# Kernel optimization log

Hardware: AMD Instinct MI355X
Metric: run time of the kernel (lower is better)

## Reference

```python
import jax, jax.numpy as jnp
import numpy as np

B, S, D = 2, 2048, 768
E, TOP_K = 8, 2
H = 4 * D  # expert hidden dim


def setup_inputs() -> dict:
    key = jax.random.key(0)
    ks = jax.random.split(key, 8)
    s_in = 1.0 / np.sqrt(D)
    s_h = 1.0 / np.sqrt(H)
    return {
        "x": jax.random.normal(ks[0], (B, S, D), dtype=jnp.float32),
        "gate_w": jax.random.uniform(ks[1], (D, E), jnp.float32, -s_in, s_in),
        "gate_b": jax.random.uniform(ks[2], (E,), jnp.float32, -s_in, s_in),
        "w1": jax.random.uniform(ks[3], (E, D, H), jnp.float32, -s_in, s_in),
        "b1": jax.random.uniform(ks[4], (E, H), jnp.float32, -s_in, s_in),
        "w2": jax.random.uniform(ks[5], (E, H, D), jnp.float32, -s_h, s_h),
        "b2": jax.random.uniform(ks[6], (E, D), jnp.float32, -s_h, s_h),
    }


def reference(x, gate_w, gate_b, w1, b1, w2, b2):
    # Router: gate linear -> top-k -> softmax over the k selected logits
    logits = jnp.einsum("bsd,de->bse", x, gate_w) + gate_b          # [B,S,E]
    top_vals, top_idx = jax.lax.top_k(logits, TOP_K)                 # [B,S,K]
    rw = jax.nn.softmax(top_vals, axis=-1)                           # [B,S,K]
    # Per-token per-expert combine weight (0 for unselected experts)
    onehot = jax.nn.one_hot(top_idx, E, dtype=x.dtype)               # [B,S,K,E]
    expert_w = jnp.einsum("bske,bsk->bse", onehot, rw)               # [B,S,E]

    # Expert MLPs (GELU exact, matching torch nn.GELU default; dropout is
    # identity in eval). Stacked as grouped GEMMs over the expert axis.
    h = jax.nn.gelu(jnp.einsum("bsd,edh->bseh", x, w1) + b1, approximate=False)
    y = jnp.einsum("bseh,ehd->bsed", h, w2) + b2                     # [B,S,E,D]
    # Weighted combine over experts
    return jnp.einsum("bse,bsed->bsd", expert_w, y)                  # [B,S,D]
```

## Files before the change

kernel.cpp:

```cpp
#include <hip/hip_runtime.h>
#include <hip/hip_bf16.h>

#define D_ 768
#define E_ 8
#define H_ 3072
#define N_TOK 4096
#define BT 64
#define BK 64

typedef _Float16 f16;
typedef f16 f16x8 __attribute__((ext_vector_type(8)));
typedef float f32x4 __attribute__((ext_vector_type(4)));

__device__ __forceinline__ void gld16(const f16* g, f16* l) {
    __builtin_amdgcn_global_load_lds(
        (const __attribute__((address_space(1))) unsigned int*)g,
        (__attribute__((address_space(3))) unsigned int*)l, 16, 0, 0);
}

__device__ __forceinline__ int prefix_off(const int* counts, int e, int* cnt_out) {
    int off = 0, cnt = 0;
#pragma unroll
    for (int q = 0; q < E_; q++) {
        int cq = counts[q];
        if (q < e) off += cq;
        if (q == e) cnt = cq;
    }
    *cnt_out = cnt;
    return off;
}

__global__ __launch_bounds__(1024) void router(const float* __restrict__ x,
                                               const float* __restrict__ gw,
                                               const float* __restrict__ gb,
                                               int* __restrict__ counts,
                                               int* __restrict__ list,
                                               float* __restrict__ wslot) {
    __shared__ int lcount[E_];
    __shared__ int lbase[E_];
    __shared__ int te0[64], te1[64], ts0[64], ts1[64];
    __shared__ float tw0[64], tw1[64];

    int tid = threadIdx.x;
    int wv = tid >> 6, lane = tid & 63;
    int s = lane >> 3, eL = lane & 7;
    if (tid < E_) lcount[tid] = 0;
    __syncthreads();

    float biasL = gb[eL];

#pragma unroll 1
    for (int i = 0; i < 4; i++) {
        int lt = wv * 4 + i;
        int tok = blockIdx.x * 64 + lt;
        const float* xr = x + (size_t)tok * D_;
        float a = 0.f;
        const float* gwl = gw + lane;
#pragma unroll 8
        for (int j = 0; j < 96; j++)
            a = fmaf(xr[j * 8 + s], gwl[j * 64], a);
        a += __shfl_xor(a, 8, 64);
        a += __shfl_xor(a, 16, 64);
        a += __shfl_xor(a, 32, 64);
        float lg = a + biasL;
        float le[8];
#pragma unroll
        for (int q = 0; q < 8; q++) le[q] = __shfl(lg, q, 64);
        float v0 = -3.4e38f, v1 = -3.4e38f;
        int i0 = 0, i1 = 0;
#pragma unroll
        for (int q = 0; q < 8; q++) {
            float l = le[q];
            if (l > v0) { v1 = v0; i1 = i0; v0 = l; i0 = q; }
            else if (l > v1) { v1 = l; i1 = q; }
        }
        if (lane == 0) {
            float p1 = expf(v1 - v0);
            float ssum = 1.f + p1;
            int s0 = atomicAdd(&lcount[i0], 1);
            int s1 = atomicAdd(&lcount[i1], 1);
            te0[lt] = i0; ts0[lt] = s0; tw0[lt] = 1.f / ssum;
            te1[lt] = i1; ts1[lt] = s1; tw1[lt] = p1 / ssum;
        }
    }
    __syncthreads();
    if (tid < E_) lbase[tid] = atomicAdd(&counts[tid], lcount[tid]);
    __syncthreads();
    if (tid < 64) {
        int tok = blockIdx.x * 64 + tid;
        int e0 = te0[tid], e1 = te1[tid];
        list[e0 * N_TOK + lbase[e0] + ts0[tid]] = tok * 2;
        list[e1 * N_TOK + lbase[e1] + ts1[tid]] = tok * 2 + 1;
        wslot[tok * 2] = tw0[tid];
        wslot[tok * 2 + 1] = tw1[tid];
    }
}

#define CVT_BLKS 9216
__global__ __launch_bounds__(256) void prep(const float* __restrict__ w1,
                                            const float* __restrict__ w2,
                                            f16* __restrict__ w1t,
                                            f16* __restrict__ w2t,
                                            const float* __restrict__ x,
                                            const int* __restrict__ counts,
                                            const int* __restrict__ list,
                                            f16* __restrict__ xg) {
    __shared__ f16 t[64][66];
    int bid = blockIdx.x;
    int tid = threadIdx.x;

    if (bid < CVT_BLKS) {
        int z = bid / 576;
        int bx = bid % 576;
        const float* src; f16* dst; int R, C, xb, yb;
        if (z < E_) {
            src = w1 + (size_t)z * D_ * H_; dst = w1t + (size_t)z * D_ * H_;
            R = D_; C = H_; xb = bx % 48; yb = bx / 48;
        } else {
            src = w2 + (size_t)(z - E_) * H_ * D_; dst = w2t + (size_t)(z - E_) * H_ * D_;
            R = H_; C = D_; xb = bx % 12; yb = bx / 12;
        }
        int r0 = yb * 64, c0 = xb * 64;
        {
            int r = tid >> 4;
            int c = (tid & 15) * 4;
#pragma unroll
            for (int i = 0; i < 4; i++) {
                float4 v = *(const float4*)(src + (size_t)(r0 + r + i * 16) * C + (c0 + c));
                t[r + i * 16][c] = (f16)v.x;
                t[r + i * 16][c + 1] = (f16)v.y;
                t[r + i * 16][c + 2] = (f16)v.z;
                t[r + i * 16][c + 3] = (f16)v.w;
            }
        }
        __syncthreads();
        {
            int c = tid >> 3;
            int rr = (tid & 7) * 8;
            int ch = rr >> 3;
#pragma unroll
            for (int i = 0; i < 2; i++) {
                int cc = c + i * 32;
                int rowi = c0 + cc;
                f16x8 o;
#pragma unroll
                for (int j = 0; j < 8; j++) o[j] = t[rr + j][cc];
                *(f16x8*)(dst + (size_t)rowi * R + r0 + (((ch ^ rowi) & 7) << 3)) = o;
            }
        }
    } else {
        int wv = tid >> 6, lane = tid & 63;
        int idx = (bid - CVT_BLKS) * 4 + wv;
        int e = idx >> 12, j = idx & (N_TOK - 1);
        int cnt;
        int off = prefix_off(counts, e, &cnt);
        if (j >= cnt) return;
        int id = list[idx];
        int row = off + j;
        const float* xr = x + (size_t)(id >> 1) * D_;
        f16* dst = xg + (size_t)row * D_;
        int r7 = row & 7;
#pragma unroll
        for (int c = 0; c < 3; c++) {
            int h = lane * 4 + c * 256;
            float4 v = *(const float4*)(xr + h);
            f16 o[4] = {(f16)v.x, (f16)v.y, (f16)v.z, (f16)v.w};
            int hs = (h & ~0x3F) | ((((h >> 3) ^ r7) & 7) << 3) | (h & 7);
            *(float2*)(dst + hs) = *(const float2*)o;
        }
    }
}

__global__ __launch_bounds__(256, 8) void gemm1(const f16* __restrict__ xg,
                                                const f16* __restrict__ w1t,
                                                const float* __restrict__ b1,
                                                const int* __restrict__ counts,
                                                f16* __restrict__ hbuf) {
    int bid = blockIdx.x;
    int e = bid & 7;
    int r = bid >> 3;
    int xb24 = r % 24;
    int yb = (r / 24) % 64;
    int xh = r / (24 * 64);
    int cnt;
    int off = prefix_off(counts, e, &cnt);
    int rb = yb * BT;
    if (rb >= cnt) return;
    int cb = (xh * 24 + xb24) * BT;

    __shared__ f16 lds[2 * BT * BK];
    char* ldsb = (char*)lds;

    int tid = threadIdx.x;
    int wv = tid >> 6, lane = tid & 63;
    int lr = lane >> 3, lc = lane & 7;

    int r0l = wv * 8 + lr;
    int r1l = 32 + wv * 8 + lr;
    int ag0 = off + rb + r0l; if (ag0 > 8191) ag0 = 8191;
    int ag1 = off + rb + r1l; if (ag1 > 8191) ag1 = 8191;
    const f16* ap0 = xg + (size_t)ag0 * D_ + lc * 8;
    const f16* ap1 = xg + (size_t)ag1 * D_ + lc * 8;
    const f16* wb = w1t + (size_t)e * H_ * D_;
    const f16* bp0 = wb + (size_t)(cb + r0l) * D_ + lc * 8;
    const f16* bp1 = wb + (size_t)(cb + r1l) * D_ + lc * 8;
    f16* la0 = lds + wv * 512;
    f16* la1 = lds + 2048 + wv * 512;
    f16* lb0 = lds + 4096 + wv * 512;
    f16* lb1 = lds + 6144 + wv * 512;

    int wr = (wv >> 1) * 32, wc = (wv & 1) * 32;
    int fr = lane & 15, qh = lane >> 4;
    int koff = (off + rb) & 7;

    int roA[2][2], roB[2][2];
#pragma unroll
    for (int m = 0; m < 2; m++)
#pragma unroll
        for (int ks = 0; ks < 2; ks++) {
            int row = wr + m * 16 + fr;
            roA[m][ks] = row * 128 + ((((ks * 4 + qh) ^ (koff + row)) & 7) << 4);
            int rwb = wc + m * 16 + fr;
            roB[m][ks] = 8192 + rwb * 128 + ((((ks * 4 + qh) ^ rwb) & 7) << 4);
        }

    f32x4 acc[2][2] = {};
    const int NT = D_ / BK;
#pragma unroll 1
    for (int t = 0; t < NT; ++t) {
        int kk = t * BK;
        gld16(ap0 + kk, la0);
        gld16(ap1 + kk, la1);
        gld16(bp0 + kk, lb0);
        gld16(bp1 + kk, lb1);
        __syncthreads();
#pragma unroll
        for (int ks = 0; ks < 2; ks++) {
            f16x8 a0 = *(const f16x8*)(ldsb + roA[0][ks]);
            f16x8 a1 = *(const f16x8*)(ldsb + roA[1][ks]);
            f16x8 b0 = *(const f16x8*)(ldsb + roB[0][ks]);
            f16x8 b1v = *(const f16x8*)(ldsb + roB[1][ks]);
            acc[0][0] = __builtin_amdgcn_mfma_f32_16x16x32_f16(a0, b0, acc[0][0], 0, 0, 0);
            acc[0][1] = __builtin_amdgcn_mfma_f32_16x16x32_f16(a0, b1v, acc[0][1], 0, 0, 0);
            acc[1][0] = __builtin_amdgcn_mfma_f32_16x16x32_f16(a1, b0, acc[1][0], 0, 0, 0);
            acc[1][1] = __builtin_amdgcn_mfma_f32_16x16x32_f16(a1, b1v, acc[1][1], 0, 0, 0);
        }
        __syncthreads();
    }

#pragma unroll
    for (int n = 0; n < 2; n++) {
        int colg = cb + wc + n * 16 + fr;
        float bias = b1[e * H_ + colg];
#pragma unroll
        for (int m = 0; m < 2; m++) {
#pragma unroll
            for (int r2 = 0; r2 < 4; r2++) {
                int j = rb + wr + m * 16 + qh * 4 + r2;
                if (j < cnt) {
                    float v = acc[m][n][r2] + bias;
                    v = 0.5f * v * (1.f + erff(v * 0.70710678f));
                    int row = off + j;
                    int hs = (colg & ~0x3F) | ((((colg >> 3) ^ row) & 7) << 3) | (colg & 7);
                    hbuf[(size_t)row * H_ + hs] = (f16)v;
                }
            }
        }
    }
}

__global__ __launch_bounds__(256, 8) void gemm2(const f16* __restrict__ hbuf,
                                                const f16* __restrict__ w2t,
                                                const float* __restrict__ b2,
                                                const int* __restrict__ counts,
                                                const int* __restrict__ list,
                                                const float* __restrict__ wslot,
                                                float* __restrict__ out) {
    int bid = blockIdx.x;
    int e = bid & 7;
    int r = bid >> 3;
    int cb12 = r % 12;
    int yb = r / 12;
    int cnt;
    int off = prefix_off(counts, e, &cnt);
    int rb = yb * BT;
    if (rb >= cnt) return;
    int cb = cb12 * BT;

    __shared__ f16 lds[2 * BT * BK];
    char* ldsb = (char*)lds;

    int tid = threadIdx.x;
    int wv = tid >> 6, lane = tid & 63;
    int lr = lane >> 3, lc = lane & 7;

    int r0l = wv * 8 + lr;
    int r1l = 32 + wv * 8 + lr;
    int ag0 = off + rb + r0l; if (ag0 > 8191) ag0 = 8191;
    int ag1 = off + rb + r1l; if (ag1 > 8191) ag1 = 8191;
    const f16* ap0 = hbuf + (size_t)ag0 * H_ + lc * 8;
    const f16* ap1 = hbuf + (size_t)ag1 * H_ + lc * 8;
    const f16* wb = w2t + (size_t)e * D_ * H_;
    const f16* bp0 = wb + (size_t)(cb + r0l) * H_ + lc * 8;
    const f16* bp1 = wb + (size_t)(cb + r1l) * H_ + lc * 8;
    f16* la0 = lds + wv * 512;
    f16* la1 = lds + 2048 + wv * 512;
    f16* lb0 = lds + 4096 + wv * 512;
    f16* lb1 = lds + 6144 + wv * 512;

    int wr = (wv >> 1) * 32, wc = (wv & 1) * 32;
    int fr = lane & 15, qh = lane >> 4;
    int koff = (off + rb) & 7;

    int roA[2][2], roB[2][2];
#pragma unroll
    for (int m = 0; m < 2; m++)
#pragma unroll
        for (int ks = 0; ks < 2; ks++) {
            int row = wr + m * 16 + fr;
            roA[m][ks] = row * 128 + ((((ks * 4 + qh) ^ (koff + row)) & 7) << 4);
            int rwb = wc + m * 16 + fr;
            roB[m][ks] = 8192 + rwb * 128 + ((((ks * 4 + qh) ^ rwb) & 7) << 4);
        }

    f32x4 acc[2][2] = {};
    const int NT = H_ / BK;
#pragma unroll 1
    for (int t = 0; t < NT; ++t) {
        int kk = t * BK;
        gld16(ap0 + kk, la0);
        gld16(ap1 + kk, la1);
        gld16(bp0 + kk, lb0);
        gld16(bp1 + kk, lb1);
        __syncthreads();
#pragma unroll
        for (int ks = 0; ks < 2; ks++) {
            f16x8 a0 = *(const f16x8*)(ldsb + roA[0][ks]);
            f16x8 a1 = *(const f16x8*)(ldsb + roA[1][ks]);
            f16x8 b0 = *(const f16x8*)(ldsb + roB[0][ks]);
            f16x8 b1v = *(const f16x8*)(ldsb + roB[1][ks]);
            acc[0][0] = __builtin_amdgcn_mfma_f32_16x16x32_f16(a0, b0, acc[0][0], 0, 0, 0);
            acc[0][1] = __builtin_amdgcn_mfma_f32_16x16x32_f16(a0, b1v, acc[0][1], 0, 0, 0);
            acc[1][0] = __builtin_amdgcn_mfma_f32_16x16x32_f16(a1, b0, acc[1][0], 0, 0, 0);
            acc[1][1] = __builtin_amdgcn_mfma_f32_16x16x32_f16(a1, b1v, acc[1][1], 0, 0, 0);
        }
        __syncthreads();
    }

#pragma unroll
    for (int n = 0; n < 2; n++) {
        int colg = cb + wc + n * 16 + fr;
        float bias = b2[e * D_ + colg];
#pragma unroll
        for (int m = 0; m < 2; m++) {
#pragma unroll
            for (int r2 = 0; r2 < 4; r2++) {
                int j = rb + wr + m * 16 + qh * 4 + r2;
                if (j < cnt) {
                    int id = list[e * N_TOK + j];
                    float w = wslot[id];
                    float v = (acc[m][n][r2] + bias) * w;
                    atomicAdd(&out[(size_t)(id >> 1) * D_ + colg], v);
                }
            }
        }
    }
}

extern "C" void kernel_launch(void* const* d_in, const int* in_sizes, int n_in,
                              void* d_out, int out_size, void* d_ws, size_t ws_size,
                              hipStream_t stream) {
    const float* x = (const float*)d_in[0];
    const float* gate_w = (const float*)d_in[1];
    const float* gate_b = (const float*)d_in[2];
    const float* w1 = (const float*)d_in[3];
    const float* b1 = (const float*)d_in[4];
    const float* w2 = (const float*)d_in[5];
    const float* b2 = (const float*)d_in[6];
    float* out = (float*)d_out;

    char* ws = (char*)d_ws;
    int* counts = (int*)ws;
    int* list = (int*)(ws + 1024);
    float* wslot = (float*)(ws + 132096);
    f16* xg = (f16*)(ws + 196608);
    f16* w1t = (f16*)(ws + 12779520);
    f16* w2t = (f16*)(ws + 50528256);
    f16* hbuf = (f16*)(ws + 88276992);

    hipMemsetAsync(counts, 0, 256, stream);
    hipMemsetAsync(out, 0, (size_t)out_size * sizeof(float), stream);

    router<<<64, 1024, 0, stream>>>(x, gate_w, gate_b, counts, list, wslot);
    prep<<<CVT_BLKS + E_ * N_TOK / 4, 256, 0, stream>>>(w1, w2, w1t, w2t, x, counts, list, xg);
    gemm1<<<E_ * 2 * 64 * 24, 256, 0, stream>>>(xg, w1t, b1, counts, hbuf);
    gemm2<<<E_ * 64 * 12, 256, 0, stream>>>(hbuf, w2t, b2, counts, list, wslot, out);
}
```

Baseline: 238.4 us.

## Double-buffer LDS tiles with async prefetch in both expert GEMMs

```diff
diff --git a/kernel.cpp b/kernel.cpp
--- a/kernel.cpp
+++ b/kernel.cpp
@@ -171,7 +171,7 @@
     }
 }
 
-__global__ __launch_bounds__(256, 8) void gemm1(const f16* __restrict__ xg,
+__global__ __launch_bounds__(256, 5) void gemm1(const f16* __restrict__ xg,
                                                 const f16* __restrict__ w1t,
                                                 const float* __restrict__ b1,
                                                 const int* __restrict__ counts,
@@ -188,8 +188,8 @@
     if (rb >= cnt) return;
     int cb = (xh * 24 + xb24) * BT;
 
-    __shared__ f16 lds[2 * BT * BK];
-    char* ldsb = (char*)lds;
+    __shared__ f16 lds[2][2 * BT * BK];
+    char* ldsb = (char*)&lds[0][0];
 
     int tid = threadIdx.x;
     int wv = tid >> 6, lane = tid & 63;
@@ -204,10 +204,10 @@
     const f16* wb = w1t + (size_t)e * H_ * D_;
     const f16* bp0 = wb + (size_t)(cb + r0l) * D_ + lc * 8;
     const f16* bp1 = wb + (size_t)(cb + r1l) * D_ + lc * 8;
-    f16* la0 = lds + wv * 512;
-    f16* la1 = lds + 2048 + wv * 512;
-    f16* lb0 = lds + 4096 + wv * 512;
-    f16* lb1 = lds + 6144 + wv * 512;
+    f16* la0 = &lds[0][0] + wv * 512;
+    f16* la1 = &lds[0][0] + 2048 + wv * 512;
+    f16* lb0 = &lds[0][0] + 4096 + wv * 512;
+    f16* lb1 = &lds[0][0] + 6144 + wv * 512;
 
     int wr = (wv >> 1) * 32, wc = (wv & 1) * 32;
     int fr = lane & 15, qh = lane >> 4;
@@ -226,26 +226,37 @@
 
     f32x4 acc[2][2] = {};
     const int NT = D_ / BK;
+
+    gld16(ap0, la0); gld16(ap1, la1); gld16(bp0, lb0); gld16(bp1, lb1);
+    gld16(ap0 + BK, la0 + 8192); gld16(ap1 + BK, la1 + 8192);
+    gld16(bp0 + BK, lb0 + 8192); gld16(bp1 + BK, lb1 + 8192);
+
 #pragma unroll 1
     for (int t = 0; t < NT; ++t) {
-        int kk = t * BK;
-        gld16(ap0 + kk, la0);
-        gld16(ap1 + kk, la1);
-        gld16(bp0 + kk, lb0);
-        gld16(bp1 + kk, lb1);
+        if (t + 1 < NT) asm volatile("s_waitcnt vmcnt(4)" ::: "memory");
+        else            asm volatile("s_waitcnt vmcnt(0)" ::: "memory");
         __syncthreads();
+        int bo = (t & 1) << 14;
 #pragma unroll
         for (int ks = 0; ks < 2; ks++) {
-            f16x8 a0 = *(const f16x8*)(ldsb + roA[0][ks]);
-            f16x8 a1 = *(const f16x8*)(ldsb + roA[1][ks]);
-            f16x8 b0 = *(const f16x8*)(ldsb + roB[0][ks]);
-            f16x8 b1v = *(const f16x8*)(ldsb + roB[1][ks]);
+            f16x8 a0 = *(const f16x8*)(ldsb + bo + roA[0][ks]);
+            f16x8 a1 = *(const f16x8*)(ldsb + bo + roA[1][ks]);
+            f16x8 b0 = *(const f16x8*)(ldsb + bo + roB[0][ks]);
+            f16x8 b1v = *(const f16x8*)(ldsb + bo + roB[1][ks]);
             acc[0][0] = __builtin_amdgcn_mfma_f32_16x16x32_f16(a0, b0, acc[0][0], 0, 0, 0);
             acc[0][1] = __builtin_amdgcn_mfma_f32_16x16x32_f16(a0, b1v, acc[0][1], 0, 0, 0);
             acc[1][0] = __builtin_amdgcn_mfma_f32_16x16x32_f16(a1, b0, acc[1][0], 0, 0, 0);
             acc[1][1] = __builtin_amdgcn_mfma_f32_16x16x32_f16(a1, b1v, acc[1][1], 0, 0, 0);
         }
         __syncthreads();
+        if (t + 2 < NT) {
+            int kk = (t + 2) * BK;
+            int ho = (t & 1) << 13;
+            gld16(ap0 + kk, la0 + ho);
+            gld16(ap1 + kk, la1 + ho);
+            gld16(bp0 + kk, lb0 + ho);
+            gld16(bp1 + kk, lb1 + ho);
+        }
     }
 
 #pragma unroll
@@ -269,7 +280,7 @@
     }
 }
 
-__global__ __launch_bounds__(256, 8) void gemm2(const f16* __restrict__ hbuf,
+__global__ __launch_bounds__(256, 5) void gemm2(const f16* __restrict__ hbuf,
                                                 const f16* __restrict__ w2t,
                                                 const float* __restrict__ b2,
                                                 const int* __restrict__ counts,
@@ -287,8 +298,8 @@
     if (rb >= cnt) return;
     int cb = cb12 * BT;
 
-    __shared__ f16 lds[2 * BT * BK];
-    char* ldsb = (char*)lds;
+    __shared__ f16 lds[2][2 * BT * BK];
+    char* ldsb = (char*)&lds[0][0];
 
     int tid = threadIdx.x;
     int wv = tid >> 6, lane = tid & 63;
@@ -303,10 +314,10 @@
     const f16* wb = w2t + (size_t)e * D_ * H_;
     const f16* bp0 = wb + (size_t)(cb + r0l) * H_ + lc * 8;
     const f16* bp1 = wb + (size_t)(cb + r1l) * H_ + lc * 8;
-    f16* la0 = lds + wv * 512;
-    f16* la1 = lds + 2048 + wv * 512;
-    f16* lb0 = lds + 4096 + wv * 512;
-    f16* lb1 = lds + 6144 + wv * 512;
+    f16* la0 = &lds[0][0] + wv * 512;
+    f16* la1 = &lds[0][0] + 2048 + wv * 512;
+    f16* lb0 = &lds[0][0] + 4096 + wv * 512;
+    f16* lb1 = &lds[0][0] + 6144 + wv * 512;
 
     int wr = (wv >> 1) * 32, wc = (wv & 1) * 32;
     int fr = lane & 15, qh = lane >> 4;
@@ -325,26 +336,37 @@
 
     f32x4 acc[2][2] = {};
     const int NT = H_ / BK;
+
+    gld16(ap0, la0); gld16(ap1, la1); gld16(bp0, lb0); gld16(bp1, lb1);
+    gld16(ap0 + BK, la0 + 8192); gld16(ap1 + BK, la1 + 8192);
+    gld16(bp0 + BK, lb0 + 8192); gld16(bp1 + BK, lb1 + 8192);
+
 #pragma unroll 1
     for (int t = 0; t < NT; ++t) {
-        int kk = t * BK;
-        gld16(ap0 + kk, la0);
-        gld16(ap1 + kk, la1);
-        gld16(bp0 + kk, lb0);
-        gld16(bp1 + kk, lb1);
+        if (t + 1 < NT) asm volatile("s_waitcnt vmcnt(4)" ::: "memory");
+        else            asm volatile("s_waitcnt vmcnt(0)" ::: "memory");
         __syncthreads();
+        int bo = (t & 1) << 14;
 #pragma unroll
         for (int ks = 0; ks < 2; ks++) {
-            f16x8 a0 = *(const f16x8*)(ldsb + roA[0][ks]);
-            f16x8 a1 = *(const f16x8*)(ldsb + roA[1][ks]);
-            f16x8 b0 = *(const f16x8*)(ldsb + roB[0][ks]);
-            f16x8 b1v = *(const f16x8*)(ldsb + roB[1][ks]);
+            f16x8 a0 = *(const f16x8*)(ldsb + bo + roA[0][ks]);
+            f16x8 a1 = *(const f16x8*)(ldsb + bo + roA[1][ks]);
+            f16x8 b0 = *(const f16x8*)(ldsb + bo + roB[0][ks]);
+            f16x8 b1v = *(const f16x8*)(ldsb + bo + roB[1][ks]);
             acc[0][0] = __builtin_amdgcn_mfma_f32_16x16x32_f16(a0, b0, acc[0][0], 0, 0, 0);
             acc[0][1] = __builtin_amdgcn_mfma_f32_16x16x32_f16(a0, b1v, acc[0][1], 0, 0, 0);
             acc[1][0] = __builtin_amdgcn_mfma_f32_16x16x32_f16(a1, b0, acc[1][0], 0, 0, 0);
             acc[1][1] = __builtin_amdgcn_mfma_f32_16x16x32_f16(a1, b1v, acc[1][1], 0, 0, 0);
         }
         __syncthreads();
+        if (t + 2 < NT) {
+            int kk = (t + 2) * BK;
+            int ho = (t & 1) << 13;
+            gld16(ap0 + kk, la0 + ho);
+            gld16(ap1 + kk, la1 + ho);
+            gld16(bp0 + kk, lb0 + ho);
+            gld16(bp1 + kk, lb1 + ho);
+        }
     }
 
 #pragma unroll
```

New measurement: 267.7 us. 1.12x slower.

## Double-buffer gemm2 LDS loads with K=32 stages and async prefetch

Applied to the files above, without the earlier changes.

```diff
diff --git a/kernel.cpp b/kernel.cpp
--- a/kernel.cpp
+++ b/kernel.cpp
@@ -287,64 +287,70 @@
     if (rb >= cnt) return;
     int cb = cb12 * BT;
 
-    __shared__ f16 lds[2 * BT * BK];
+    __shared__ f16 lds[8192];
     char* ldsb = (char*)lds;
 
     int tid = threadIdx.x;
     int wv = tid >> 6, lane = tid & 63;
-    int lr = lane >> 3, lc = lane & 7;
-
-    int r0l = wv * 8 + lr;
-    int r1l = 32 + wv * 8 + lr;
-    int ag0 = off + rb + r0l; if (ag0 > 8191) ag0 = 8191;
-    int ag1 = off + rb + r1l; if (ag1 > 8191) ag1 = 8191;
-    const f16* ap0 = hbuf + (size_t)ag0 * H_ + lc * 8;
-    const f16* ap1 = hbuf + (size_t)ag1 * H_ + lc * 8;
-    const f16* wb = w2t + (size_t)e * D_ * H_;
-    const f16* bp0 = wb + (size_t)(cb + r0l) * H_ + lc * 8;
-    const f16* bp1 = wb + (size_t)(cb + r1l) * H_ + lc * 8;
-    f16* la0 = lds + wv * 512;
-    f16* la1 = lds + 2048 + wv * 512;
-    f16* lb0 = lds + 4096 + wv * 512;
-    f16* lb1 = lds + 6144 + wv * 512;
+
+    int rs = tid >> 2;
+    int ps = tid & 3;
+    int q2s = ((ps - (rs >> 2)) & 3) ^ (rs & 3);
+    int agA = off + rb + rs; if (agA > 8191) agA = 8191;
+    int posAe = q2s ^ (agA & 7);
+    const f16* gA_e = hbuf + (size_t)agA * H_ + posAe * 8;
+    const f16* gA_o = hbuf + (size_t)agA * H_ + (posAe ^ 4) * 8;
+    int grB = cb + rs;
+    int posBe = q2s ^ (rs & 7);
+    const f16* gB_e = w2t + (size_t)e * D_ * H_ + (size_t)grB * H_ + posBe * 8;
+    const f16* gB_o = w2t + (size_t)e * D_ * H_ + (size_t)grB * H_ + (posBe ^ 4) * 8;
+    f16* ldA = lds + wv * 512;
+    f16* ldB = lds + 2048 + wv * 512;
 
     int wr = (wv >> 1) * 32, wc = (wv & 1) * 32;
     int fr = lane & 15, qh = lane >> 4;
-    int koff = (off + rb) & 7;
-
-    int roA[2][2], roB[2][2];
-#pragma unroll
-    for (int m = 0; m < 2; m++)
-#pragma unroll
-        for (int ks = 0; ks < 2; ks++) {
-            int row = wr + m * 16 + fr;
-            roA[m][ks] = row * 128 + ((((ks * 4 + qh) ^ (koff + row)) & 7) << 4);
-            int rwb = wc + m * 16 + fr;
-            roB[m][ks] = 8192 + rwb * 128 + ((((ks * 4 + qh) ^ rwb) & 7) << 4);
-        }
+
+    int roA[2], roB[2];
+#pragma unroll
+    for (int m = 0; m < 2; m++) {
+        int rl = wr + m * 16 + fr;
+        int p = (((qh ^ (rl & 3)) + (rl >> 2)) & 3);
+        roA[m] = rl * 64 + p * 16;
+        int rlb = wc + m * 16 + fr;
+        int pb = (((qh ^ (rlb & 3)) + (rlb >> 2)) & 3);
+        roB[m] = 4096 + rlb * 64 + pb * 16;
+    }
+
+#define G2STG(tt, b) do {                                              \
+    int g64 = ((tt) >> 1) * 64;                                        \
+    const f16* pa_ = (((tt) & 1) ? gA_o : gA_e) + g64;                 \
+    const f16* pb_ = (((tt) & 1) ? gB_o : gB_e) + g64;                 \
+    gld16(pa_, ldA + (b) * 4096);                                      \
+    gld16(pb_, ldB + (b) * 4096);                                      \
+} while (0)
 
     f32x4 acc[2][2] = {};
-    const int NT = H_ / BK;
+    const int NT = H_ / 32;
+
+    G2STG(0, 0);
+    G2STG(1, 1);
+
 #pragma unroll 1
     for (int t = 0; t < NT; ++t) {
-        int kk = t * BK;
-        gld16(ap0 + kk, la0);
-        gld16(ap1 + kk, la1);
-        gld16(bp0 + kk, lb0);
-        gld16(bp1 + kk, lb1);
+        if (t + 1 < NT) asm volatile("s_waitcnt vmcnt(2)" ::: "memory");
+        else            asm volatile("s_waitcnt vmcnt(0)" ::: "memory");
         __syncthreads();
-#pragma unroll
-        for (int ks = 0; ks < 2; ks++) {
-            f16x8 a0 = *(const f16x8*)(ldsb + roA[0][ks]);
-            f16x8 a1 = *(const f16x8*)(ldsb + roA[1][ks]);
-            f16x8 b0 = *(const f16x8*)(ldsb + roB[0][ks]);
-            f16x8 b1v = *(const f16x8*)(ldsb + roB[1][ks]);
-            acc[0][0] = __builtin_amdgcn_mfma_f32_16x16x32_f16(a0, b0, acc[0][0], 0, 0, 0);
-            acc[0][1] = __builtin_amdgcn_mfma_f32_16x16x32_f16(a0, b1v, acc[0][1], 0, 0, 0);
-            acc[1][0] = __builtin_amdgcn_mfma_f32_16x16x32_f16(a1, b0, acc[1][0], 0, 0, 0);
-            acc[1][1] = __builtin_amdgcn_mfma_f32_16x16x32_f16(a1, b1v, acc[1][1], 0, 0, 0);
-        }
+        int bo = (t & 1) << 13;
+        f16x8 a0 = *(const f16x8*)(ldsb + bo + roA[0]);
+        f16x8 a1 = *(const f16x8*)(ldsb + bo + roA[1]);
+        f16x8 b0 = *(const f16x8*)(ldsb + bo + roB[0]);
+        f16x8 b1v = *(const f16x8*)(ldsb + bo + roB[1]);
+        acc[0][0] = __builtin_amdgcn_mfma_f32_16x16x32_f16(a0, b0, acc[0][0], 0, 0, 0);
+        acc[0][1] = __builtin_amdgcn_mfma_f32_16x16x32_f16(a0, b1v, acc[0][1], 0, 0, 0);
+        acc[1][0] = __builtin_amdgcn_mfma_f32_16x16x32_f16(a1, b0, acc[1][0], 0, 0, 0);
+        acc[1][1] = __builtin_amdgcn_mfma_f32_16x16x32_f16(a1, b1v, acc[1][1], 0, 0, 0);
         __syncthreads();
+        if (t + 2 < NT) G2STG(t + 2, t & 1);
     }
 
 #pragma unroll
```

New measurement: 272.1 us. 1.14x slower.
